# Kernel tuning notes

Measured on AMD Instinct MI355X. Metric: run time of the kernel, lower is better.

The kernel has to match this reference:

```python
import jax, jax.numpy as jnp
import numpy as np

GX, GY, NH = 480, 360, 32
EPS = 1e-5


def _bn(x, g, b):
    # torch BatchNorm1d training-mode stats over the point dimension
    m = jnp.mean(x, axis=0)
    v = jnp.mean((x - m) ** 2, axis=0)
    return g * (x - m) / jnp.sqrt(v + EPS) + b


def setup_inputs():
    key = jax.random.key(0)
    ks = jax.random.split(key, 24)
    B, N, F = 2, 120000, 7
    s = 0.02
    inp = {
        "pt_fea": jax.random.normal(ks[0], (B, N, F), jnp.float32),
        "xy_ind": jax.random.randint(ks[1], (B, N, 2), 0, 360, dtype=jnp.int32),
        "bn0_g": jnp.ones((7,), jnp.float32), "bn0_b": jnp.zeros((7,), jnp.float32),
        "W1": jax.random.normal(ks[2], (7, 64), jnp.float32) * s,  "b1": jnp.zeros((64,), jnp.float32),
        "bn1_g": jnp.ones((64,), jnp.float32), "bn1_b": jnp.zeros((64,), jnp.float32),
        "W2": jax.random.normal(ks[3], (64, 128), jnp.float32) * s, "b2": jnp.zeros((128,), jnp.float32),
        "bn2_g": jnp.ones((128,), jnp.float32), "bn2_b": jnp.zeros((128,), jnp.float32),
        "W3": jax.random.normal(ks[4], (128, 256), jnp.float32) * s, "b3": jnp.zeros((256,), jnp.float32),
        "bn3_g": jnp.ones((256,), jnp.float32), "bn3_b": jnp.zeros((256,), jnp.float32),
        "W4": jax.random.normal(ks[5], (256, 512), jnp.float32) * s, "b4": jnp.zeros((512,), jnp.float32),
        "W5": jax.random.normal(ks[6], (512, NH), jnp.float32) * s, "b5": jnp.zeros((NH,), jnp.float32),
    }
    return inp


def _forward_sample(fea, xy, bn0_g, bn0_b, W1, b1, bn1_g, bn1_b, W2, b2,
                    bn2_g, bn2_b, W3, b3, bn3_g, bn3_b, W4, b4, W5, b5):
    # Simplified PointNet: BN -> (Linear, BN, ReLU) x3 -> Linear
    x = _bn(fea, bn0_g, bn0_b)
    x = jax.nn.relu(_bn(x @ W1 + b1, bn1_g, bn1_b))
    x = jax.nn.relu(_bn(x @ W2 + b2, bn2_g, bn2_b))
    x = jax.nn.relu(_bn(x @ W3 + b3, bn3_g, bn3_b))
    x = x @ W4 + b4                              # [N, 512]
    # per-voxel segment max over flattened BEV cell id
    ids = xy[:, 0] * GY + xy[:, 1]               # [N]
    nseg = GX * GY
    seg = jax.ops.segment_max(x, ids, num_segments=nseg)   # [nseg, 512]
    cnt = jax.ops.segment_sum(jnp.ones(ids.shape[0], x.dtype), ids, num_segments=nseg)
    occ = (cnt > 0)[:, None]
    seg = jnp.where(occ, seg, 0.0)               # empty voxels -> 0 (scatter semantics)
    nh = jax.nn.relu(seg @ W5 + b5)              # fea_compression
    nh = jnp.where(occ, nh, 0.0)
    return nh.reshape(GX, GY, NH).transpose(2, 0, 1)  # [NH, GX, GY]


def reference(pt_fea, xy_ind, bn0_g, bn0_b, W1, b1, bn1_g, bn1_b, W2, b2,
              bn2_g, bn2_b, W3, b3, bn3_g, bn3_b, W4, b4, W5, b5):
    f = lambda fea, xy: _forward_sample(fea, xy, bn0_g, bn0_b, W1, b1, bn1_g, bn1_b,
                                        W2, b2, bn2_g, bn2_b, W3, b3, bn3_g, bn3_b,
                                        W4, b4, W5, b5)
    return jax.vmap(f)(pt_fea, xy_ind)           # [B, NH, GX, GY]
```

## Files before the change

### kernel.cpp

```cpp
#include <hip/hip_runtime.h>
#include <cstdint>

#define GXD 480
#define GYD 360
#define NHD 32
#define NPTS 120000
#define MPAD 120064
#define SEGR 129600
#define NSEG (GXD*GYD)
#define EPSB 1e-5f

using short8 = __attribute__((ext_vector_type(8))) short;
using f32x4  = __attribute__((ext_vector_type(4))) float;

__device__ __forceinline__ float bf2f(unsigned short u) {
    return __uint_as_float(((unsigned int)u) << 16);
}
__device__ __forceinline__ unsigned short f2bf(float f) {
    unsigned int u = __float_as_uint(f);
    u += 0x7fffu + ((u >> 16) & 1u);
    return (unsigned short)(u >> 16);
}
__device__ __forceinline__ unsigned int bnrelu_pack(unsigned int wv, float sc0, float sh0,
                                                    float sc1, float sh1)
{
    float lo = __uint_as_float(wv << 16);
    float hi = __uint_as_float(wv & 0xffff0000u);
    lo = fmaxf(fmaf(lo, sc0, sh0), 0.f);
    hi = fmaxf(fmaf(hi, sc1, sh1), 0.f);
    unsigned int r;
    asm("v_cvt_pk_bf16_f32 %0, %1, %2" : "=v"(r) : "v"(lo), "v"(hi));
    return r;
}

__device__ __forceinline__ void async16(const unsigned short* g, unsigned short* l)
{
    __builtin_amdgcn_global_load_lds(
        (const __attribute__((address_space(1))) unsigned int*)g,
        (__attribute__((address_space(3))) unsigned int*)l, 16, 0, 0);
}

__global__ __launch_bounds__(256) void bn0_stats_kernel(
    const float* __restrict__ fea, float* __restrict__ s0, float* __restrict__ q0)
{
    float s[7] = {0,0,0,0,0,0,0}, q[7] = {0,0,0,0,0,0,0};
    for (int p = blockIdx.x * 256 + threadIdx.x; p < NPTS; p += gridDim.x * 256) {
        const float* r = fea + (size_t)p * 7;
#pragma unroll
        for (int f = 0; f < 7; ++f) { float v = r[f]; s[f] += v; q[f] += v * v; }
    }
    __shared__ float red[256];
    int t = threadIdx.x;
#pragma unroll
    for (int f = 0; f < 7; ++f) {
        red[t] = s[f]; __syncthreads();
        for (int o = 128; o > 0; o >>= 1) {
            if (t < o) red[t] += red[t + o];
            __syncthreads();
        }
        if (t == 0) atomicAdd(&s0[f], red[0]);
        __syncthreads();
        red[t] = q[f]; __syncthreads();
        for (int o = 128; o > 0; o >>= 1) {
            if (t < o) red[t] += red[t + o];
            __syncthreads();
        }
        if (t == 0) atomicAdd(&q0[f], red[0]);
        __syncthreads();
    }
}

__global__ void prep0_kernel(const float* __restrict__ s0, const float* __restrict__ q0,
                             const float* __restrict__ g0, const float* __restrict__ b0,
                             const float* __restrict__ W1, const float* __restrict__ b1,
                             float* __restrict__ W1p, float* __restrict__ b1p)
{
    __shared__ float sc[7], sh[7];
    int t = threadIdx.x;
    if (t < 7) {
        float m = s0[t] / (float)NPTS;
        float v = q0[t] / (float)NPTS - m * m;
        float inv = 1.0f / sqrtf(fmaxf(v, 0.f) + EPSB);
        sc[t] = g0[t] * inv;
        sh[t] = b0[t] - m * g0[t] * inv;
    }
    __syncthreads();
    if (t < 64) {
        float acc = b1[t];
#pragma unroll
        for (int f = 0; f < 7; ++f) {
            W1p[f * 64 + t] = W1[f * 64 + t] * sc[f];
            acc += sh[f] * W1[f * 64 + t];
        }
        b1p[t] = acc;
    }
}

__global__ void prep_bn_kernel(const float* __restrict__ sum, const float* __restrict__ sq,
                               const float* __restrict__ g, const float* __restrict__ b,
                               float* __restrict__ sc, float* __restrict__ sh, int C)
{
    int c = blockIdx.x * blockDim.x + threadIdx.x;
    if (c < C) {
        float m = sum[c] / (float)NPTS;
        float v = sq[c] / (float)NPTS - m * m;
        float inv = 1.0f / sqrtf(fmaxf(v, 0.f) + EPSB);
        sc[c] = g[c] * inv;
        sh[c] = b[c] - m * g[c] * inv;
    }
}

template<int C>
__global__ __launch_bounds__(256) void bnrelu_kernel(
    unsigned short* __restrict__ Y,
    const float* __restrict__ sc, const float* __restrict__ sh)
{
    __shared__ float scs[C], shs[C];
    int t = threadIdx.x;
    for (int i = t; i < C; i += 256) { scs[i] = sc[i]; shs[i] = sh[i]; }
    __syncthreads();
    const size_t total8 = (size_t)MPAD * C / 8;
    for (size_t i = (size_t)blockIdx.x * 256 + t; i < total8; i += (size_t)gridDim.x * 256) {
        int c0 = (int)((i * 8) & (size_t)(C - 1));
        uint4 v = *(const uint4*)(Y + i * 8);
        float4 s0 = *(const float4*)&scs[c0];
        float4 s1 = *(const float4*)&scs[c0 + 4];
        float4 h0 = *(const float4*)&shs[c0];
        float4 h1 = *(const float4*)&shs[c0 + 4];
        uint4 o;
        o.x = bnrelu_pack(v.x, s0.x, h0.x, s0.y, h0.y);
        o.y = bnrelu_pack(v.y, s0.z, h0.z, s0.w, h0.w);
        o.z = bnrelu_pack(v.z, s1.x, h1.x, s1.y, h1.y);
        o.w = bnrelu_pack(v.w, s1.z, h1.z, s1.w, h1.w);
        *(uint4*)(Y + i * 8) = o;
    }
}

__global__ __launch_bounds__(256) void wtrans_kernel(const float* __restrict__ W,
                                                     unsigned short* __restrict__ Wt,
                                                     int K, int N)
{
    int i = blockIdx.x * 256 + threadIdx.x;
    if (i < K * N) {
        int k = i / N, n = i % N;
        Wt[(size_t)n * K + k] = f2bf(W[i]);
    }
}

__global__ __launch_bounds__(256) void layer1_kernel(
    const float* __restrict__ fea, const float* __restrict__ W1p, const float* __restrict__ b1p,
    unsigned short* __restrict__ y1, float* __restrict__ sum1, float* __restrict__ sq1)
{
    __shared__ float Wl[448], bl[64];
    __shared__ float feaL[256 * 7];
    __shared__ float colsum[64], colsq[64];
    int t = threadIdx.x;
    int p0 = blockIdx.x * 256;
    for (int i = t; i < 448; i += 256) Wl[i] = W1p[i];
    if (t < 64) { bl[t] = b1p[t]; colsum[t] = 0.f; colsq[t] = 0.f; }
    int nval7 = (NPTS - p0) * 7;
    for (int i = t; i < 256 * 7; i += 256)
        feaL[i] = (i < nval7) ? fea[(size_t)p0 * 7 + i] : 0.f;
    __syncthreads();
    int cg = t & 7, pt = t >> 3;
    float s[8] = {}, q[8] = {};
#pragma unroll
    for (int it = 0; it < 8; ++it) {
        int row = it * 32 + pt;
        bool valid = (p0 + row) < NPTS;
        float f[7];
#pragma unroll
        for (int ff = 0; ff < 7; ++ff) f[ff] = feaL[row * 7 + ff];
        float vj[8];
#pragma unroll
        for (int j = 0; j < 8; ++j) {
            int c = cg * 8 + j;
            float v = bl[c];
#pragma unroll
            for (int ff = 0; ff < 7; ++ff) v = fmaf(f[ff], Wl[ff * 64 + c], v);
            vj[j] = v;
            if (valid) { s[j] += v; q[j] += v * v; }
        }
        uint4 ow;
        ow.x = (unsigned int)f2bf(vj[0]) | ((unsigned int)f2bf(vj[1]) << 16);
        ow.y = (unsigned int)f2bf(vj[2]) | ((unsigned int)f2bf(vj[3]) << 16);
        ow.z = (unsigned int)f2bf(vj[4]) | ((unsigned int)f2bf(vj[5]) << 16);
        ow.w = (unsigned int)f2bf(vj[6]) | ((unsigned int)f2bf(vj[7]) << 16);
        *(uint4*)(y1 + (size_t)(p0 + row) * 64 + cg * 8) = ow;
    }
#pragma unroll
    for (int off = 8; off < 64; off <<= 1) {
#pragma unroll
        for (int j = 0; j < 8; ++j) {
            s[j] += __shfl_xor(s[j], off);
            q[j] += __shfl_xor(q[j], off);
        }
    }
    if ((t & 63) < 8) {
#pragma unroll
        for (int j = 0; j < 8; ++j) {
            atomicAdd(&colsum[cg * 8 + j], s[j]);
            atomicAdd(&colsq[cg * 8 + j], q[j]);
        }
    }
    __syncthreads();
    if (t < 64) {
        atomicAdd(&sum1[t], colsum[t]);
        atomicAdd(&sq1[t], colsq[t]);
    }
}

template<int K, int NC, bool STATS>
__global__ __launch_bounds__(256) void gemm_quad(
    const unsigned short* __restrict__ A, const unsigned short* __restrict__ Wt,
    const float* __restrict__ bias, unsigned short* __restrict__ Y,
    float* __restrict__ osum, float* __restrict__ osq)
{
    __shared__ __align__(16) unsigned short lds[4 * 8192];
    __shared__ float colsum[128], colsq[128];
    int t = threadIdx.x;
    int w = t >> 6, ln = t & 63, quad = ln >> 4, lr = ln & 15;
    int wr = w >> 1, wc = w & 1;
    int mb = blockIdx.y * 128 + wr * 64;
    int cb = blockIdx.x * 128 + wc * 64;
    unsigned short* A0 = lds + w * 8192;
    unsigned short* B0 = A0 + 2048;
    unsigned short* A1 = A0 + 4096;
    unsigned short* B1 = A0 + 6144;

    if (STATS && t < 128) { colsum[t] = 0.f; colsq[t] = 0.f; }
    __syncthreads();

    const int grow = ln >> 2;
    const int koff = (ln & 3) * 8;

    f32x4 acc[4][4];
#pragma unroll
    for (int i = 0; i < 4; ++i)
#pragma unroll
        for (int j = 0; j < 4; ++j) acc[i][j] = (f32x4){0.f, 0.f, 0.f, 0.f};

#pragma unroll
    for (int i = 0; i < 4; ++i) {
        async16(A  + (size_t)(mb + i * 16 + grow) * K + koff, A0 + i * 512 + ln * 8);
        async16(Wt + (size_t)(cb + i * 16 + grow) * K + koff, B0 + i * 512 + ln * 8);
    }
#pragma unroll
    for (int i = 0; i < 4; ++i) {
        async16(A  + (size_t)(mb + i * 16 + grow) * K + 32 + koff, A1 + i * 512 + ln * 8);
        async16(Wt + (size_t)(cb + i * 16 + grow) * K + 32 + koff, B1 + i * 512 + ln * 8);
    }

#pragma unroll
    for (int r = 0; r < K / 32; ++r) {
        const int kt = r * 32;
        unsigned short* Acur = (r & 1) ? A1 : A0;
        unsigned short* Bcur = (r & 1) ? B1 : B0;
        if (r + 1 < K / 32)
            asm volatile("s_waitcnt vmcnt(8)" ::: "memory");
        else
            asm volatile("s_waitcnt vmcnt(0)" ::: "memory");
        short8 af[4], bfr[4];
#pragma unroll
        for (int mi = 0; mi < 4; ++mi)
            af[mi] = *(const short8*)&Acur[mi * 512 + lr * 32 + quad * 8];
#pragma unroll
        for (int ni = 0; ni < 4; ++ni)
            bfr[ni] = *(const short8*)&Bcur[ni * 512 + lr * 32 + quad * 8];
        asm volatile("s_waitcnt lgkmcnt(0)" ::: "memory");
        if (r + 2 < K / 32) {
            const int kn = kt + 64;
#pragma unroll
            for (int i = 0; i < 4; ++i) {
                async16(A  + (size_t)(mb + i * 16 + grow) * K + kn + koff,
                        Acur + i * 512 + ln * 8);
                async16(Wt + (size_t)(cb + i * 16 + grow) * K + kn + koff,
                        Bcur + i * 512 + ln * 8);
            }
        }
#pragma unroll
        for (int mi = 0; mi < 4; ++mi)
#pragma unroll
            for (int ni = 0; ni < 4; ++ni)
                acc[mi][ni] = __builtin_amdgcn_mfma_f32_16x16x32_bf16(
                    af[mi], bfr[ni], acc[mi][ni], 0, 0, 0);
    }

    unsigned short* Cw = A0;
#pragma unroll
    for (int ni = 0; ni < 4; ++ni) {
        int col = ni * 16 + lr;
        float bv = bias[cb + col];
        float s = 0.f, q = 0.f;
#pragma unroll
        for (int mi = 0; mi < 4; ++mi) {
            int rb = mi * 16 + quad * 4;
#pragma unroll
            for (int r = 0; r < 4; ++r) {
                float v = acc[mi][ni][r] + bv;
                Cw[(rb + r) * 64 + col] = f2bf(v);
                if (STATS && (mb + rb + r) < NPTS) { s += v; q += v * v; }
            }
        }
        if (STATS) {
            atomicAdd(&colsum[wc * 64 + col], s);
            atomicAdd(&colsq[wc * 64 + col], q);
        }
    }
#pragma unroll
    for (int i = 0; i < 8; ++i) {
        int idx = i * 64 + ln;
        int row = idx >> 3, colq = (idx & 7) * 8;
        *(uint4*)(Y + (size_t)(mb + row) * NC + cb + colq) = *(const uint4*)&Cw[row * 64 + colq];
    }
    if (STATS) {
        __syncthreads();
        if (t < 128) {
            atomicAdd(&osum[blockIdx.x * 128 + t], colsum[t]);
            atomicAdd(&osq[blockIdx.x * 128 + t], colsq[t]);
        }
    }
}

__global__ __launch_bounds__(256) void hist_kernel(const int* __restrict__ xy,
                                                   int* __restrict__ cnt)
{
    int p = blockIdx.x * 256 + threadIdx.x;
    if (p < NPTS) {
        int id = xy[(size_t)p * 2] * GYD + xy[(size_t)p * 2 + 1];
        atomicAdd(&cnt[id], 1);
    }
}

__global__ __launch_bounds__(256) void scanA_kernel(const int* __restrict__ cnt,
                                                    int* __restrict__ csum)
{
    __shared__ int red[256];
    int t = threadIdx.x, base = blockIdx.x * 2048;
    int s = 0;
    for (int i = t; i < 2048; i += 256) {
        int idx = base + i;
        if (idx < SEGR) s += cnt[idx];
    }
    red[t] = s; __syncthreads();
    for (int o = 128; o > 0; o >>= 1) { if (t < o) red[t] += red[t + o]; __syncthreads(); }
    if (t == 0) csum[blockIdx.x] = red[0];
}

__global__ void scanB_kernel(int* __restrict__ csum, int* __restrict__ offs)
{
    if (threadIdx.x == 0) {
        int run = 0;
        for (int i = 0; i < 64; ++i) { int v = csum[i]; csum[i] = run; run += v; }
        offs[SEGR] = run;
    }
}

__global__ __launch_bounds__(256) void scanC_kernel(const int* __restrict__ cnt,
                                                    const int* __restrict__ csum,
                                                    int* __restrict__ offs,
                                                    int* __restrict__ cursor)
{
    __shared__ int red[256];
    int t = threadIdx.x, base = blockIdx.x * 2048;
    int v[8]; int s = 0;
#pragma unroll
    for (int i = 0; i < 8; ++i) {
        int idx = base + t * 8 + i;
        v[i] = (idx < SEGR) ? cnt[idx] : 0;
        s += v[i];
    }
    red[t] = s; __syncthreads();
    for (int o = 1; o < 256; o <<= 1) {
        int x = (t >= o) ? red[t - o] : 0;
        __syncthreads();
        red[t] += x;
        __syncthreads();
    }
    int run = red[t] - s + csum[blockIdx.x];
#pragma unroll
    for (int i = 0; i < 8; ++i) {
        int idx = base + t * 8 + i;
        if (idx < SEGR) { offs[idx] = run; cursor[idx] = run; }
        run += v[i];
    }
}

__global__ __launch_bounds__(256) void scatter_idx_kernel(const int* __restrict__ xy,
                                                          int* __restrict__ cursor,
                                                          int* __restrict__ order)
{
    int p = blockIdx.x * 256 + threadIdx.x;
    if (p < NPTS) {
        int id = xy[(size_t)p * 2] * GYD + xy[(size_t)p * 2 + 1];
        int pos = atomicAdd(&cursor[id], 1);
        order[pos] = p;
    }
}

__global__ __launch_bounds__(256) void segmax_l5_kernel(
    const unsigned short* __restrict__ y4g, const unsigned short* __restrict__ Wt5,
    const int* __restrict__ offs, const int* __restrict__ order,
    int g, float* __restrict__ E)
{
    __shared__ __align__(16) unsigned short seg[64 * 136];
    __shared__ __align__(16) unsigned short w5s[32 * 136];
    __shared__ int offs_s[65];
    int t = threadIdx.x;
    int c0 = blockIdx.x * 64;
    if (t < 65) offs_s[t] = offs[c0 + t];
    {
        int n = t >> 3, ko = (t & 7) * 16;
        *(uint4*)&w5s[n * 136 + ko]     = *(const uint4*)(Wt5 + (size_t)n * 512 + g * 128 + ko);
        *(uint4*)&w5s[n * 136 + ko + 8] = *(const uint4*)(Wt5 + (size_t)n * 512 + g * 128 + ko + 8);
    }
    __syncthreads();
    int cell = t >> 2, q = t & 3;
    float mx[32];
#pragma unroll
    for (int i = 0; i < 32; ++i) mx[i] = -3.0e38f;
    int jb = offs_s[cell], je = offs_s[cell + 1];
    for (int j = jb; j < je; ++j) {
        int p = order[j];
        const uint4* rp = (const uint4*)(y4g + (size_t)p * 128 + q * 32);
#pragma unroll
        for (int u = 0; u < 4; ++u) {
            uint4 vv = rp[u];
            unsigned int wv[4] = {vv.x, vv.y, vv.z, vv.w};
#pragma unroll
            for (int k2 = 0; k2 < 4; ++k2) {
                int idx = u * 8 + k2 * 2;
                mx[idx]     = fmaxf(mx[idx],     bf2f((unsigned short)(wv[k2] & 0xffffu)));
                mx[idx + 1] = fmaxf(mx[idx + 1], bf2f((unsigned short)(wv[k2] >> 16)));
            }
        }
    }
    bool empty = (jb == je);
#pragma unroll
    for (int i = 0; i < 16; ++i) {
        float lo = empty ? 0.f : mx[2 * i], hi = empty ? 0.f : mx[2 * i + 1];
        unsigned int pk = (unsigned int)f2bf(lo) | ((unsigned int)f2bf(hi) << 16);
        *(unsigned int*)&seg[cell * 136 + q * 32 + 2 * i] = pk;
    }
    __syncthreads();
    int lane = t & 63, w = t >> 6, quad = lane >> 4, lr = lane & 15;
    f32x4 acc[2];
    acc[0] = (f32x4){0.f, 0.f, 0.f, 0.f};
    acc[1] = (f32x4){0.f, 0.f, 0.f, 0.f};
#pragma unroll
    for (int kt = 0; kt < 4; ++kt) {
        short8 af = *(const short8*)&seg[(w * 16 + lr) * 136 + kt * 32 + quad * 8];
#pragma unroll
        for (int ni = 0; ni < 2; ++ni) {
            short8 bfr = *(const short8*)&w5s[(ni * 16 + lr) * 136 + kt * 32 + quad * 8];
            acc[ni] = __builtin_amdgcn_mfma_f32_16x16x32_bf16(af, bfr, acc[ni], 0, 0, 0);
        }
    }
#pragma unroll
    for (int ni = 0; ni < 2; ++ni) {
        int h = ni * 16 + lr;
#pragma unroll
        for (int r = 0; r < 4; ++r) {
            int cr = w * 16 + quad * 4 + r;
            float* ep = E + (size_t)(c0 + cr) * 32 + h;
            float v = acc[ni][r];
            if (g > 0) v += *ep;
            *ep = v;
        }
    }
}

__global__ __launch_bounds__(256) void out_kernel(
    const float* __restrict__ E, const int* __restrict__ cnt,
    const float* __restrict__ b5, float* __restrict__ out)
{
    int t = threadIdx.x;
    int c0 = blockIdx.x * 64;
    int lane = t & 63, hq = t >> 6;
    int cell = c0 + lane;
    if (c0 >= SEGR) {
#pragma unroll
        for (int j = 0; j < 8; ++j)
            out[(size_t)(hq * 8 + j) * NSEG + cell] = 0.f;
        return;
    }
    bool oc = cnt[cell] > 0;
    float4 e0 = *(const float4*)(E + (size_t)cell * 32 + hq * 8);
    float4 e1 = *(const float4*)(E + (size_t)cell * 32 + hq * 8 + 4);
    float r[8] = {e0.x, e0.y, e0.z, e0.w, e1.x, e1.y, e1.z, e1.w};
#pragma unroll
    for (int j = 0; j < 8; ++j) {
        float v = oc ? fmaxf(r[j] + b5[hq * 8 + j], 0.f) : 0.f;
        out[(size_t)(hq * 8 + j) * NSEG + cell] = v;
    }
}

extern "C" void kernel_launch(void* const* d_in, const int* in_sizes, int n_in,
                              void* d_out, int out_size, void* d_ws, size_t ws_size,
                              hipStream_t stream)
{
    const float* pt_fea = (const float*)d_in[0];
    const int*   xy_ind = (const int*)d_in[1];
    const float* bn0_g  = (const float*)d_in[2];
    const float* bn0_b  = (const float*)d_in[3];
    const float* W1     = (const float*)d_in[4];
    const float* b1     = (const float*)d_in[5];
    const float* bn1_g  = (const float*)d_in[6];
    const float* bn1_b  = (const float*)d_in[7];
    const float* W2     = (const float*)d_in[8];
    const float* b2     = (const float*)d_in[9];
    const float* bn2_g  = (const float*)d_in[10];
    const float* bn2_b  = (const float*)d_in[11];
    const float* W3     = (const float*)d_in[12];
    const float* b3     = (const float*)d_in[13];
    const float* bn3_g  = (const float*)d_in[14];
    const float* bn3_b  = (const float*)d_in[15];
    const float* W4     = (const float*)d_in[16];
    const float* b4     = (const float*)d_in[17];
    const float* W5     = (const float*)d_in[18];
    const float* b5     = (const float*)d_in[19];
    float* out = (float*)d_out;

    const size_t oY2   = 61472768;
    const size_t oE    = oY2 + (size_t)MPAD * 128 * 2;
    const size_t oCnt  = oE + (size_t)SEGR * 32 * 4;
    const size_t oOffs = oCnt + 518400;
    const size_t oCur  = oOffs + 518528;
    const size_t oOrd  = oCur + 518400;
    const size_t oCsum = oOrd + 480000;
    const size_t oSt   = oCsum + 512;
    const size_t oWt2  = oSt + 16384;
    const size_t oWt3  = oWt2 + 16384;
    const size_t oWt4  = oWt3 + 65536;
    const size_t oWt5  = oWt4 + 262144;

    unsigned short* y1   = (unsigned short*)d_ws;
    unsigned short* y3   = (unsigned short*)d_ws;
    unsigned short* y2   = (unsigned short*)((char*)d_ws + oY2);
    unsigned short* y4g  = (unsigned short*)((char*)d_ws + oY2);
    float*          E    = (float*)((char*)d_ws + oE);
    int*            cnt  = (int*)((char*)d_ws + oCnt);
    int*            offs = (int*)((char*)d_ws + oOffs);
    int*            cur  = (int*)((char*)d_ws + oCur);
    int*            ord  = (int*)((char*)d_ws + oOrd);
    int*            csum = (int*)((char*)d_ws + oCsum);
    float*          st   = (float*)((char*)d_ws + oSt);
    unsigned short* Wt2  = (unsigned short*)((char*)d_ws + oWt2);
    unsigned short* Wt3  = (unsigned short*)((char*)d_ws + oWt3);
    unsigned short* Wt4  = (unsigned short*)((char*)d_ws + oWt4);
    unsigned short* Wt5  = (unsigned short*)((char*)d_ws + oWt5);

    float* s0 = st + 0;     float* q0 = st + 8;
    float* W1p = st + 16;   float* b1p = st + 464;
    float* sum1 = st + 528; float* sq1 = st + 592; float* sc1 = st + 656; float* sh1 = st + 720;
    float* sum2 = st + 784; float* sq2 = st + 912; float* sc2 = st + 1040; float* sh2 = st + 1168;
    float* sum3 = st + 1296; float* sq3 = st + 1552; float* sc3 = st + 1808; float* sh3 = st + 2064;

    const int MB128 = MPAD / 128;

    wtrans_kernel<<<(64 * 128 + 255) / 256, 256, 0, stream>>>(W2, Wt2, 64, 128);
    wtrans_kernel<<<(128 * 256 + 255) / 256, 256, 0, stream>>>(W3, Wt3, 128, 256);
    wtrans_kernel<<<(256 * 512 + 255) / 256, 256, 0, stream>>>(W4, Wt4, 256, 512);
    wtrans_kernel<<<(512 * 32 + 255) / 256, 256, 0, stream>>>(W5, Wt5, 512, 32);

    for (int b = 0; b < 2; ++b) {
        const float* fea_b = pt_fea + (size_t)b * NPTS * 7;
        const int*   xy_b  = xy_ind + (size_t)b * NPTS * 2;
        float*       out_b = out + (size_t)b * NHD * NSEG;

        (void)hipMemsetAsync(st, 0, 2320 * sizeof(float), stream);
        (void)hipMemsetAsync(cnt, 0, (size_t)SEGR * 4, stream);

        bn0_stats_kernel<<<128, 256, 0, stream>>>(fea_b, s0, q0);
        prep0_kernel<<<1, 64, 0, stream>>>(s0, q0, bn0_g, bn0_b, W1, b1, W1p, b1p);
        layer1_kernel<<<MPAD / 256, 256, 0, stream>>>(fea_b, W1p, b1p, y1, sum1, sq1);
        prep_bn_kernel<<<1, 64, 0, stream>>>(sum1, sq1, bn1_g, bn1_b, sc1, sh1, 64);
        bnrelu_kernel<64><<<1024, 256, 0, stream>>>(y1, sc1, sh1);
        gemm_quad<64, 128, true><<<dim3(1, MB128), 256, 0, stream>>>(
            y1, Wt2, b2, y2, sum2, sq2);
        prep_bn_kernel<<<1, 128, 0, stream>>>(sum2, sq2, bn2_g, bn2_b, sc2, sh2, 128);
        bnrelu_kernel<128><<<2048, 256, 0, stream>>>(y2, sc2, sh2);
        gemm_quad<128, 256, true><<<dim3(2, MB128), 256, 0, stream>>>(
            y2, Wt3, b3, y3, sum3, sq3);
        prep_bn_kernel<<<1, 256, 0, stream>>>(sum3, sq3, bn3_g, bn3_b, sc3, sh3, 256);
        bnrelu_kernel<256><<<2048, 256, 0, stream>>>(y3, sc3, sh3);

        hist_kernel<<<(NPTS + 255) / 256, 256, 0, stream>>>(xy_b, cnt);
        scanA_kernel<<<64, 256, 0, stream>>>(cnt, csum);
        scanB_kernel<<<1, 64, 0, stream>>>(csum, offs);
        scanC_kernel<<<64, 256, 0, stream>>>(cnt, csum, offs, cur);
        scatter_idx_kernel<<<(NPTS + 255) / 256, 256, 0, stream>>>(xy_b, cur, ord);

        for (int g = 0; g < 4; ++g) {
            gemm_quad<256, 128, false><<<dim3(1, MB128), 256, 0, stream>>>(
                y3, Wt4 + (size_t)g * 128 * 256, b4 + g * 128, y4g,
                nullptr, nullptr);
            segmax_l5_kernel<<<SEGR / 64, 256, 0, stream>>>(y4g, Wt5, offs, ord, g, E);
        }
        out_kernel<<<NSEG / 64, 256, 0, stream>>>(E, cnt, b5, out_b);
    }
}
```

Before: 847.4 us.

## Share A/B tiles across waves in block-level LDS for gemm_quad

```diff
diff --git a/kernel.cpp b/kernel.cpp
--- a/kernel.cpp
+++ b/kernel.cpp
@@ -216,68 +216,62 @@
     const float* __restrict__ bias, unsigned short* __restrict__ Y,
     float* __restrict__ osum, float* __restrict__ osq)
 {
-    __shared__ __align__(16) unsigned short lds[4 * 8192];
+    __shared__ __align__(16) unsigned short lds[16384];
     __shared__ float colsum[128], colsq[128];
     int t = threadIdx.x;
     int w = t >> 6, ln = t & 63, quad = ln >> 4, lr = ln & 15;
     int wr = w >> 1, wc = w & 1;
-    int mb = blockIdx.y * 128 + wr * 64;
-    int cb = blockIdx.x * 128 + wc * 64;
-    unsigned short* A0 = lds + w * 8192;
-    unsigned short* B0 = A0 + 2048;
-    unsigned short* A1 = A0 + 4096;
-    unsigned short* B1 = A0 + 6144;
+    const int mbase = blockIdx.y * 128;
+    const int cbase = blockIdx.x * 128;
+    unsigned short* Asl = lds;
+    unsigned short* Bsl = lds + 8192;
 
     if (STATS && t < 128) { colsum[t] = 0.f; colsq[t] = 0.f; }
     __syncthreads();
 
-    const int grow = ln >> 2;
+    const int srow = w * 16 + (ln >> 2);
     const int koff = (ln & 3) * 8;
 
+    auto stage = [&](int buf, int kt) {
+#pragma unroll
+        for (int half = 0; half < 2; ++half) {
+            int row = half * 64 + srow;
+            async16(A  + (size_t)(mbase + row) * K + kt + koff,
+                    Asl + buf * 4096 + half * 2048 + w * 512 + ln * 8);
+            async16(Wt + (size_t)(cbase + row) * K + kt + koff,
+                    Bsl + buf * 4096 + half * 2048 + w * 512 + ln * 8);
+        }
+    };
+
     f32x4 acc[4][4];
 #pragma unroll
     for (int i = 0; i < 4; ++i)
 #pragma unroll
         for (int j = 0; j < 4; ++j) acc[i][j] = (f32x4){0.f, 0.f, 0.f, 0.f};
 
-#pragma unroll
-    for (int i = 0; i < 4; ++i) {
-        async16(A  + (size_t)(mb + i * 16 + grow) * K + koff, A0 + i * 512 + ln * 8);
-        async16(Wt + (size_t)(cb + i * 16 + grow) * K + koff, B0 + i * 512 + ln * 8);
-    }
-#pragma unroll
-    for (int i = 0; i < 4; ++i) {
-        async16(A  + (size_t)(mb + i * 16 + grow) * K + 32 + koff, A1 + i * 512 + ln * 8);
-        async16(Wt + (size_t)(cb + i * 16 + grow) * K + 32 + koff, B1 + i * 512 + ln * 8);
-    }
-
-#pragma unroll
-    for (int r = 0; r < K / 32; ++r) {
-        const int kt = r * 32;
-        unsigned short* Acur = (r & 1) ? A1 : A0;
-        unsigned short* Bcur = (r & 1) ? B1 : B0;
-        if (r + 1 < K / 32)
-            asm volatile("s_waitcnt vmcnt(8)" ::: "memory");
+    stage(0, 0);
+    stage(1, 32);
+
+    constexpr int NR = K / 32;
+#pragma unroll
+    for (int r = 0; r < NR; ++r) {
+        const int buf = r & 1;
+        if (r + 1 < NR)
+            asm volatile("s_waitcnt vmcnt(4)" ::: "memory");
         else
             asm volatile("s_waitcnt vmcnt(0)" ::: "memory");
+        asm volatile("s_barrier" ::: "memory");
         short8 af[4], bfr[4];
 #pragma unroll
         for (int mi = 0; mi < 4; ++mi)
-            af[mi] = *(const short8*)&Acur[mi * 512 + lr * 32 + quad * 8];
+            af[mi] = *(const short8*)&Asl[buf * 4096 + (wr * 64 + mi * 16 + lr) * 32 + quad * 8];
 #pragma unroll
         for (int ni = 0; ni < 4; ++ni)
-            bfr[ni] = *(const short8*)&Bcur[ni * 512 + lr * 32 + quad * 8];
+            bfr[ni] = *(const short8*)&Bsl[buf * 4096 + (wc * 64 + ni * 16 + lr) * 32 + quad * 8];
         asm volatile("s_waitcnt lgkmcnt(0)" ::: "memory");
-        if (r + 2 < K / 32) {
-            const int kn = kt + 64;
-#pragma unroll
-            for (int i = 0; i < 4; ++i) {
-                async16(A  + (size_t)(mb + i * 16 + grow) * K + kn + koff,
-                        Acur + i * 512 + ln * 8);
-                async16(Wt + (size_t)(cb + i * 16 + grow) * K + kn + koff,
-                        Bcur + i * 512 + ln * 8);
-            }
-        }
+        asm volatile("s_barrier" ::: "memory");
+        if (r + 2 < NR)
+            stage(buf, (r + 2) * 32);
 #pragma unroll
         for (int mi = 0; mi < 4; ++mi)
 #pragma unroll
@@ -285,12 +279,13 @@
                 acc[mi][ni] = __builtin_amdgcn_mfma_f32_16x16x32_bf16(
                     af[mi], bfr[ni], acc[mi][ni], 0, 0, 0);
     }
-
-    unsigned short* Cw = A0;
+    __syncthreads();
+
+    unsigned short* Cw = lds + w * 4096;
 #pragma unroll
     for (int ni = 0; ni < 4; ++ni) {
         int col = ni * 16 + lr;
-        float bv = bias[cb + col];
+        float bv = bias[cbase + wc * 64 + col];
         float s = 0.f, q = 0.f;
 #pragma unroll
         for (int mi = 0; mi < 4; ++mi) {
@@ -299,7 +294,7 @@
             for (int r = 0; r < 4; ++r) {
                 float v = acc[mi][ni][r] + bv;
                 Cw[(rb + r) * 64 + col] = f2bf(v);
-                if (STATS && (mb + rb + r) < NPTS) { s += v; q += v * v; }
+                if (STATS && (mbase + wr * 64 + rb + r) < NPTS) { s += v; q += v * v; }
             }
         }
         if (STATS) {
@@ -311,7 +306,8 @@
     for (int i = 0; i < 8; ++i) {
         int idx = i * 64 + ln;
         int row = idx >> 3, colq = (idx & 7) * 8;
-        *(uint4*)(Y + (size_t)(mb + row) * NC + cb + colq) = *(const uint4*)&Cw[row * 64 + colq];
+        *(uint4*)(Y + (size_t)(mbase + wr * 64 + row) * NC + cbase + wc * 64 + colq) =
+            *(const uint4*)&Cw[row * 64 + colq];
     }
     if (STATS) {
         __syncthreads();
```

Result: faster. 809.2 us (-4.5%).
